# Performance work log

Hardware: AMD Instinct MI355X
Metric: run time of the kernel (lower is better)

Reference implementation:

```python
import jax, jax.numpy as jnp
import numpy as np

ETA = 0.1
DT = 1.0
H, DH = 8, 64


def setup_inputs() -> dict:
    key = jax.random.key(0)
    ks = jax.random.split(key, 7)
    B, N, D = 4, 2048, 1024
    s = 0.02
    return {
        "x": jax.random.normal(ks[0], (B, N, D), dtype=jnp.float32),
        "gamma": jax.random.uniform(ks[1], (B, N), dtype=jnp.float32),
        "state": jnp.zeros((B, H, DH, DH), dtype=jnp.float32),
        "Wq": (jax.random.normal(ks[2], (D, H * DH), dtype=jnp.float32) * s),
        "Wk": (jax.random.normal(ks[3], (D, H * DH), dtype=jnp.float32) * s),
        "Wv": (jax.random.normal(ks[4], (D, H * DH), dtype=jnp.float32) * s),
        "Wo": (jax.random.normal(ks[5], (H * DH, D), dtype=jnp.float32) * s),
        "bo": jnp.zeros((D,), dtype=jnp.float32),
    }


def reference(x, gamma, state, Wq, Wk, Wv, Wo, bo):
    B, N, D = x.shape
    # projections -> (N, B, H, DH) for scan over time
    q = (x @ Wq).reshape(B, N, H, DH).transpose(1, 0, 2, 3)
    k = (x @ Wk).reshape(B, N, H, DH).transpose(1, 0, 2, 3)
    v = (x @ Wv).reshape(B, N, H, DH).transpose(1, 0, 2, 3)
    # decay = exp(-clamp(gamma*dt, max=10)) -> (N, B)
    decay = jnp.exp(-jnp.minimum(gamma * DT, 10.0)).T

    def step(st, inp):
        q_t, k_t, v_t, d_t = inp  # (B,H,DH),(B,H,DH),(B,H,DH),(B,)
        # W_new = exp(-Gamma*dt) * stop_grad(W_old) + eta * k^T v
        st_new = d_t[:, None, None, None] * jax.lax.stop_gradient(st) \
                 + ETA * jnp.einsum('bhi,bhj->bhij', k_t, v_t)
        y_t = jnp.einsum('bhij,bhj->bhi', st_new, q_t)  # (B,H,DH)
        return st_new, y_t

    state_final, ys = jax.lax.scan(step, state, (q, k, v, decay))
    # ys: (N, B, H, DH) -> (B, N, H*DH)
    y = ys.transpose(1, 0, 2, 3).reshape(B, N, H * DH)
    out = y @ Wo + bo
    return out, state_final
```

## Files before the change

kernel.cpp:

```cpp
#include <hip/hip_runtime.h>

#define ETA 0.1f
#define BATCH 4
#define SEQ 2048
#define DMODEL 1024
#define NH 8
#define DHEAD 64
#define HD 512
#define QKVW 1536
#define CH 64
#define NCH (SEQ / CH)

typedef float f32x4 __attribute__((ext_vector_type(4)));
typedef short short8 __attribute__((ext_vector_type(8)));
typedef short short4v __attribute__((ext_vector_type(4)));

static __device__ __forceinline__ ushort f2bf(float f) {
  union { float f; unsigned u; } x; x.f = f;
  unsigned r = (x.u + 0x7fffu + ((x.u >> 16) & 1u)) >> 16;
  return (ushort)r;
}
static __device__ __forceinline__ float bf2f(ushort u) {
  union { unsigned u; float f; } x; x.u = ((unsigned)u) << 16;
  return x.f;
}

#define GLDS16(g, l)                                                    \
  __builtin_amdgcn_global_load_lds(                                     \
      (const __attribute__((address_space(1))) unsigned int*)(const void*)(g), \
      (__attribute__((address_space(3))) unsigned int*)(void*)(l), 16, 0, 0)

__global__ __launch_bounds__(256) void convx_kernel(
    const float* __restrict__ x, ushort* __restrict__ xb) {
  size_t i = ((size_t)blockIdx.x * 256 + threadIdx.x) * 16;
  ushort t[16];
#pragma unroll
  for (int u = 0; u < 4; ++u) {
    f32x4 v = *(const f32x4*)&x[i + u * 4];
#pragma unroll
    for (int e = 0; e < 4; ++e) t[u * 4 + e] = f2bf(v[e]);
  }
  *(short8*)&xb[i] = *(short8*)&t[0];
  *(short8*)&xb[i + 8] = *(short8*)&t[8];
}

__global__ __launch_bounds__(256) void convw_kernel(
    const float* __restrict__ Wq, const float* __restrict__ Wk,
    const float* __restrict__ Wv, const float* __restrict__ Wo,
    ushort* __restrict__ Wt, ushort* __restrict__ Wot) {
  const int m = blockIdx.y;
  const int bx = blockIdx.x;
  const int tid = threadIdx.x;
  __shared__ float T[32][33];

  const float* src;
  ushort* dst;
  int srcN, dstK, k0, n0, rowOff;
  if (m < 3) {
    src = (m == 0) ? Wq : ((m == 1) ? Wk : Wv);
    srcN = 512; dstK = 1024;
    k0 = (bx >> 4) << 5; n0 = (bx & 15) << 5;
    dst = Wt; rowOff = m * 512;
  } else {
    src = Wo; srcN = 1024; dstK = 512;
    k0 = (bx >> 5) << 5; n0 = (bx & 31) << 5;
    dst = Wot; rowOff = 0;
  }
  const int r = tid >> 3, c4 = (tid & 7) << 2;
  f32x4 v = *(const f32x4*)&src[(size_t)(k0 + r) * srcN + n0 + c4];
  T[r][c4 + 0] = v[0]; T[r][c4 + 1] = v[1];
  T[r][c4 + 2] = v[2]; T[r][c4 + 3] = v[3];
  __syncthreads();
  short4v o;
#pragma unroll
  for (int e = 0; e < 4; ++e) o[e] = (short)f2bf(T[c4 + e][r]);
  *(short4v*)&dst[(size_t)(rowOff + n0 + r) * dstK + k0 + c4] = o;
}

template <bool OUT_BF16>
__global__ __launch_bounds__(256, 3) void gemm_bt_kernel(
    const ushort* __restrict__ A, const ushort* __restrict__ Bt,
    void* __restrict__ Cv, const float* __restrict__ bias,
    int M, int N, int K) {
  const int tiles_n = N >> 7;
  const int nwg = gridDim.x;
  const int bid = blockIdx.x;
  const int swz = (bid & 7) * (nwg >> 3) + (bid >> 3);
  const int bm = swz / tiles_n;
  const int bn = swz % tiles_n;
  const int tid = threadIdx.x;
  const int w = tid >> 6, lane = tid & 63;
  const int wr = w >> 1, wc = w & 1;
  const int fr = lane & 15, fq = lane >> 4;

  __shared__ ushort As[3][128][32];
  __shared__ ushort Bs[3][128][32];

  f32x4 acc[4][4];
#pragma unroll
  for (int mi = 0; mi < 4; ++mi)
#pragma unroll
    for (int ni = 0; ni < 4; ++ni) acc[mi][ni] = f32x4{0.f, 0.f, 0.f, 0.f};

  const int lw = lane >> 2;
  const int scz = ((lane & 3) ^ ((lane >> 3) & 3)) << 3;
  const ushort* ga = A + (size_t)(bm * 128 + w * 32 + lw) * K + scz;
  const ushort* gb = Bt + (size_t)(bn * 128 + w * 32 + lw) * K + scz;
  const size_t rstep = (size_t)16 * K;

  const int nt = K >> 5;

#pragma unroll
  for (int pt = 0; pt < 2; ++pt) {
    ushort* la = &As[pt][w * 32][0];
    ushort* lb = &Bs[pt][w * 32][0];
    GLDS16(ga + pt * 32, la);
    GLDS16(ga + pt * 32 + rstep, la + 512);
    GLDS16(gb + pt * 32, lb);
    GLDS16(gb + pt * 32 + rstep, lb + 512);
  }

  const int fqs8 = (fq ^ ((fr >> 1) & 3)) * 8;

  for (int t = 0; t < nt; ++t) {
    if (t < nt - 1) {
      asm volatile("s_waitcnt vmcnt(4) lgkmcnt(0)\n\ts_barrier" ::: "memory");
    } else {
      asm volatile("s_waitcnt vmcnt(0) lgkmcnt(0)\n\ts_barrier" ::: "memory");
    }
    if (t + 2 < nt) {
      const int sb = (t + 2) % 3;
      const int kt = (t + 2) << 5;
      ushort* la = &As[sb][w * 32][0];
      ushort* lb = &Bs[sb][w * 32][0];
      GLDS16(ga + kt, la);
      GLDS16(ga + kt + rstep, la + 512);
      GLDS16(gb + kt, lb);
      GLDS16(gb + kt + rstep, lb + 512);
    }
    const int cb = t % 3;
    short8 a[4], b[4];
#pragma unroll
    for (int mi = 0; mi < 4; ++mi)
      a[mi] = *(const short8*)&As[cb][wr * 64 + mi * 16 + fr][fqs8];
#pragma unroll
    for (int ni = 0; ni < 4; ++ni)
      b[ni] = *(const short8*)&Bs[cb][wc * 64 + ni * 16 + fr][fqs8];
#pragma unroll
    for (int mi = 0; mi < 4; ++mi)
#pragma unroll
      for (int ni = 0; ni < 4; ++ni)
        acc[mi][ni] = __builtin_amdgcn_mfma_f32_16x16x32_bf16(
            a[mi], b[ni], acc[mi][ni], 0, 0, 0);
  }

#pragma unroll
  for (int ni = 0; ni < 4; ++ni) {
    const int gc = bn * 128 + wc * 64 + ni * 16 + fr;
    float badd = (!OUT_BF16 && bias) ? bias[gc] : 0.f;
#pragma unroll
    for (int mi = 0; mi < 4; ++mi) {
#pragma unroll
      for (int r = 0; r < 4; ++r) {
        const int gr = bm * 128 + wr * 64 + mi * 16 + fq * 4 + r;
        if (OUT_BF16) {
          ((ushort*)Cv)[(size_t)gr * N + gc] = f2bf(acc[mi][ni][r]);
        } else {
          ((float*)Cv)[(size_t)gr * N + gc] = acc[mi][ni][r] + badd;
        }
      }
    }
  }
}

__global__ __launch_bounds__(256) void intra_kernel(
    const ushort* __restrict__ qkv, const float* __restrict__ gamma,
    ushort* __restrict__ ybf, ushort* __restrict__ S, float* __restrict__ clb) {
  const int bx = blockIdx.x;
  const int c = bx & (NCH - 1);
  const int h = (bx >> 5) & (NH - 1);
  const int b = bx >> 8;
  const int tid = threadIdx.x;
  const int w = tid >> 6, lane = tid & 63;
  const int fr = lane & 15, fq = lane >> 4;

  __shared__ ushort Qs[64][72];
  __shared__ ushort Vs[64][72];
  __shared__ ushort KT[64][72];
  __shared__ ushort VT[64][72];
  __shared__ ushort Ps[64][72];
  __shared__ float cumS[64];
  __shared__ float clS;

  const int p = tid >> 2, d0 = (tid & 3) * 16;
  const ushort* base = &qkv[((size_t)b * SEQ + c * CH + p) * QKVW + h * 64 + d0];
  short8 q0 = *(const short8*)base;
  short8 q1 = *(const short8*)(base + 8);
  short8 k0 = *(const short8*)(base + 512);
  short8 k1 = *(const short8*)(base + 520);
  short8 v0 = *(const short8*)(base + 1024);
  short8 v1 = *(const short8*)(base + 1032);

  if (tid < 64) {
    float g = gamma[(size_t)b * SEQ + c * CH + tid];
    float prod = expf(-fminf(g, 10.f));
#pragma unroll
    for (int off = 1; off < 64; off <<= 1) {
      float o = __shfl_up(prod, off);
      if (tid >= off) prod *= o;
    }
    cumS[tid] = prod;
    if (tid == 63) clS = prod;
  }
  __syncthreads();

  {
    const float cp = cumS[p];
    const float rc = 1.f / cp;
    ushort tq[16], tv[16];
#pragma unroll
    for (int j = 0; j < 8; ++j) {
      tq[j]     = f2bf(bf2f((ushort)q0[j]) * cp);
      tq[8 + j] = f2bf(bf2f((ushort)q1[j]) * cp);
      tv[j]     = f2bf(bf2f((ushort)v0[j]) * rc);
      tv[8 + j] = f2bf(bf2f((ushort)v1[j]) * rc);
      KT[d0 + j][p] = (ushort)k0[j];
      KT[d0 + 8 + j][p] = (ushort)k1[j];
      VT[d0 + j][p] = tv[j];
      VT[d0 + 8 + j][p] = tv[8 + j];
    }
    *(short8*)&Qs[p][d0] = *(short8*)&tq[0];
    *(short8*)&Qs[p][d0 + 8] = *(short8*)&tq[8];
    *(short8*)&Vs[p][d0] = *(short8*)&tv[0];
    *(short8*)&Vs[p][d0 + 8] = *(short8*)&tv[8];
  }
  __syncthreads();

  const int arow = w * 16 + fr;
  {
    short8 a0 = *(const short8*)&Qs[arow][fq * 8];
    short8 a1 = *(const short8*)&Qs[arow][32 + fq * 8];
#pragma unroll
    for (int cf = 0; cf < 4; ++cf) {
      f32x4 acc = {0.f, 0.f, 0.f, 0.f};
      if (cf <= w) {
        short8 b0 = *(const short8*)&Vs[cf * 16 + fr][fq * 8];
        short8 b1 = *(const short8*)&Vs[cf * 16 + fr][32 + fq * 8];
        acc = __builtin_amdgcn_mfma_f32_16x16x32_bf16(a0, b0, acc, 0, 0, 0);
        acc = __builtin_amdgcn_mfma_f32_16x16x32_bf16(a1, b1, acc, 0, 0, 0);
      }
#pragma unroll
      for (int r = 0; r < 4; ++r) {
        int pi = w * 16 + fq * 4 + r, si = cf * 16 + fr;
        Ps[pi][si] = f2bf((si <= pi) ? acc[r] * ETA : 0.f);
      }
    }
  }
  __syncthreads();

  {
    short8 p0 = *(const short8*)&Ps[arow][fq * 8];
    short8 p1 = *(const short8*)&Ps[arow][32 + fq * 8];
    short8 ka0 = *(const short8*)&KT[arow][fq * 8];
    short8 ka1 = *(const short8*)&KT[arow][32 + fq * 8];
    const float scl = ETA * clS;
    const size_t yrow0 = (size_t)b * SEQ + c * CH;
    ushort* Sp = &S[(((size_t)(b * NH + h)) * NCH + c) << 12];
#pragma unroll
    for (int cf = 0; cf < 4; ++cf) {
      short8 bk0 = *(const short8*)&KT[cf * 16 + fr][fq * 8];
      short8 bk1 = *(const short8*)&KT[cf * 16 + fr][32 + fq * 8];
      f32x4 accY = {0.f, 0.f, 0.f, 0.f};
      accY = __builtin_amdgcn_mfma_f32_16x16x32_bf16(p0, bk0, accY, 0, 0, 0);
      accY = __builtin_amdgcn_mfma_f32_16x16x32_bf16(p1, bk1, accY, 0, 0, 0);
      short8 bv0 = *(const short8*)&VT[cf * 16 + fr][fq * 8];
      short8 bv1 = *(const short8*)&VT[cf * 16 + fr][32 + fq * 8];
      f32x4 accS = {0.f, 0.f, 0.f, 0.f};
      accS = __builtin_amdgcn_mfma_f32_16x16x32_bf16(ka0, bv0, accS, 0, 0, 0);
      accS = __builtin_amdgcn_mfma_f32_16x16x32_bf16(ka1, bv1, accS, 0, 0, 0);
#pragma unroll
      for (int r = 0; r < 4; ++r) {
        int row = w * 16 + fq * 4 + r;
        int col = cf * 16 + fr;
        ybf[(yrow0 + row) * HD + h * 64 + col] = f2bf(accY[r]);
        Sp[row * 64 + col] = f2bf(accS[r] * scl);
      }
    }
  }
  if (tid == 0 && h == 0) clb[b * NCH + c] = clS;
}

__global__ __launch_bounds__(256) void prop_kernel(
    const float* __restrict__ state0, const ushort* __restrict__ S,
    const float* __restrict__ clb, ushort* __restrict__ stash,
    float* __restrict__ state_out) {
  const int bh = blockIdx.x >> 2, rg = blockIdx.x & 3;
  const int b = bh >> 3;
  const int tid = threadIdx.x;
  const int i = rg * 16 + (tid >> 4);
  const int j0 = (tid & 15) * 4;
  const size_t off = ((size_t)bh * 64 + i) * 64 + j0;
  const size_t coff = (size_t)i * 64 + j0;

  f32x4 st = *(const f32x4*)&state0[off];
#pragma unroll 4
  for (int c = 0; c < NCH; ++c) {
    const size_t base = (((size_t)bh * NCH + c) << 12) + coff;
    short4v sv;
#pragma unroll
    for (int e = 0; e < 4; ++e) sv[e] = (short)f2bf(st[e]);
    *(short4v*)&stash[base] = sv;
    short4v s = *(const short4v*)&S[base];
    float clv = clb[b * NCH + c];
#pragma unroll
    for (int e = 0; e < 4; ++e) st[e] = st[e] * clv + bf2f((ushort)s[e]);
  }
  *(f32x4*)&state_out[off] = st;
}

__global__ __launch_bounds__(256) void inter_kernel(
    const ushort* __restrict__ qkv, const float* __restrict__ gamma,
    const ushort* __restrict__ stash, ushort* __restrict__ ybf) {
  const int bx = blockIdx.x;
  const int c = bx & (NCH - 1);
  const int h = (bx >> 5) & (NH - 1);
  const int b = bx >> 8;
  const int tid = threadIdx.x;
  const int w = tid >> 6, lane = tid & 63;
  const int fr = lane & 15, fq = lane >> 4;

  __shared__ ushort Qs[64][72];
  __shared__ ushort Bs[64][72];
  __shared__ float cumS[64];

  const int p = tid >> 2, d0 = (tid & 3) * 16;
  const ushort* qp = &qkv[((size_t)b * SEQ + c * CH + p) * QKVW + h * 64 + d0];
  short8 q0 = *(const short8*)qp;
  short8 q1 = *(const short8*)(qp + 8);
  const size_t sb = ((((size_t)(b * NH + h)) * NCH + c) << 12) + (size_t)p * 64 + d0;
  short8 s0 = *(const short8*)&stash[sb];
  short8 s1 = *(const short8*)&stash[sb + 8];

  if (tid < 64) {
    float g = gamma[(size_t)b * SEQ + c * CH + tid];
    float prod = expf(-fminf(g, 10.f));
#pragma unroll
    for (int off = 1; off < 64; off <<= 1) {
      float o = __shfl_up(prod, off);
      if (tid >= off) prod *= o;
    }
    cumS[tid] = prod;
  }
  __syncthreads();

  {
    const float cp = cumS[p];
    ushort tq[16];
#pragma unroll
    for (int j = 0; j < 8; ++j) {
      tq[j]     = f2bf(bf2f((ushort)q0[j]) * cp);
      tq[8 + j] = f2bf(bf2f((ushort)q1[j]) * cp);
    }
    *(short8*)&Qs[p][d0] = *(short8*)&tq[0];
    *(short8*)&Qs[p][d0 + 8] = *(short8*)&tq[8];
    *(short8*)&Bs[p][d0] = s0;
    *(short8*)&Bs[p][d0 + 8] = s1;
  }
  __syncthreads();

  const int arow = w * 16 + fr;
  short8 a0 = *(const short8*)&Qs[arow][fq * 8];
  short8 a1 = *(const short8*)&Qs[arow][32 + fq * 8];
  const size_t yrow0 = (size_t)b * SEQ + c * CH;
#pragma unroll
  for (int cf = 0; cf < 4; ++cf) {
    short8 b0 = *(const short8*)&Bs[cf * 16 + fr][fq * 8];
    short8 b1 = *(const short8*)&Bs[cf * 16 + fr][32 + fq * 8];
    f32x4 acc = {0.f, 0.f, 0.f, 0.f};
    acc = __builtin_amdgcn_mfma_f32_16x16x32_bf16(a0, b0, acc, 0, 0, 0);
    acc = __builtin_amdgcn_mfma_f32_16x16x32_bf16(a1, b1, acc, 0, 0, 0);
#pragma unroll
    for (int r = 0; r < 4; ++r) {
      int row = w * 16 + fq * 4 + r;
      int col = cf * 16 + fr;
      size_t idx = (yrow0 + row) * HD + h * 64 + col;
      ybf[idx] = f2bf(bf2f(ybf[idx]) + acc[r]);
    }
  }
}

extern "C" void kernel_launch(void* const* d_in, const int* in_sizes, int n_in,
                              void* d_out, int out_size, void* d_ws, size_t ws_size,
                              hipStream_t stream) {
  const float* x      = (const float*)d_in[0];
  const float* gamma  = (const float*)d_in[1];
  const float* state0 = (const float*)d_in[2];
  const float* Wq     = (const float*)d_in[3];
  const float* Wk     = (const float*)d_in[4];
  const float* Wv     = (const float*)d_in[5];
  const float* Wo     = (const float*)d_in[6];
  const float* bo     = (const float*)d_in[7];

  float* out = (float*)d_out;
  float* state_out = out + (size_t)BATCH * SEQ * DMODEL;

  const int M = BATCH * SEQ;

  ushort* xb  = (ushort*)d_ws;
  ushort* wt  = xb + (size_t)M * DMODEL;
  ushort* wot = wt + (size_t)QKVW * DMODEL;
  ushort* qkv = wot + (size_t)DMODEL * HD;
  ushort* ybf = qkv + (size_t)M * QKVW;
  ushort* Sb  = ybf + (size_t)M * HD;
  ushort* stash = Sb + (size_t)BATCH * NH * NCH * 4096;
  float*  clb   = (float*)(stash + (size_t)BATCH * NH * NCH * 4096);

  dim3 blk(256);

  convx_kernel<<<dim3((M * DMODEL) / (256 * 16)), blk, 0, stream>>>(x, xb);
  convw_kernel<<<dim3(512, 4), blk, 0, stream>>>(Wq, Wk, Wv, Wo, wt, wot);

  gemm_bt_kernel<true><<<dim3((M / 128) * (QKVW / 128)), blk, 0, stream>>>(
      xb, wt, qkv, nullptr, M, QKVW, DMODEL);

  intra_kernel<<<dim3(BATCH * NH * NCH), blk, 0, stream>>>(
      qkv, gamma, ybf, Sb, clb);
  prop_kernel<<<dim3(BATCH * NH * 4), blk, 0, stream>>>(
      state0, Sb, clb, stash, state_out);
  inter_kernel<<<dim3(BATCH * NH * NCH), blk, 0, stream>>>(
      qkv, gamma, stash, ybf);

  gemm_bt_kernel<false><<<dim3((M / 128) * (DMODEL / 128)), blk, 0, stream>>>(
      ybf, wot, out, bo, M, DMODEL, HD);
}
```

Measured before the change: 96.70 us.

## Move intra-chunk output into inter kernel and merge conversion kernels

```diff
diff --git a/kernel.cpp b/kernel.cpp
--- a/kernel.cpp
+++ b/kernel.cpp
@@ -30,29 +30,29 @@
       (const __attribute__((address_space(1))) unsigned int*)(const void*)(g), \
       (__attribute__((address_space(3))) unsigned int*)(void*)(l), 16, 0, 0)
 
-__global__ __launch_bounds__(256) void convx_kernel(
-    const float* __restrict__ x, ushort* __restrict__ xb) {
-  size_t i = ((size_t)blockIdx.x * 256 + threadIdx.x) * 16;
-  ushort t[16];
-#pragma unroll
-  for (int u = 0; u < 4; ++u) {
-    f32x4 v = *(const f32x4*)&x[i + u * 4];
-#pragma unroll
-    for (int e = 0; e < 4; ++e) t[u * 4 + e] = f2bf(v[e]);
-  }
-  *(short8*)&xb[i] = *(short8*)&t[0];
-  *(short8*)&xb[i + 8] = *(short8*)&t[8];
-}
-
-__global__ __launch_bounds__(256) void convw_kernel(
-    const float* __restrict__ Wq, const float* __restrict__ Wk,
-    const float* __restrict__ Wv, const float* __restrict__ Wo,
+__global__ __launch_bounds__(256) void conv_kernel(
+    const float* __restrict__ x, const float* __restrict__ Wq,
+    const float* __restrict__ Wk, const float* __restrict__ Wv,
+    const float* __restrict__ Wo, ushort* __restrict__ xb,
     ushort* __restrict__ Wt, ushort* __restrict__ Wot) {
-  const int m = blockIdx.y;
-  const int bx = blockIdx.x;
   const int tid = threadIdx.x;
   __shared__ float T[32][33];
-
+  if (blockIdx.x < 2048) {
+    size_t i = ((size_t)blockIdx.x * 256 + tid) * 16;
+    ushort t[16];
+#pragma unroll
+    for (int u = 0; u < 4; ++u) {
+      f32x4 v = *(const f32x4*)&x[i + u * 4];
+#pragma unroll
+      for (int e = 0; e < 4; ++e) t[u * 4 + e] = f2bf(v[e]);
+    }
+    *(short8*)&xb[i] = *(short8*)&t[0];
+    *(short8*)&xb[i + 8] = *(short8*)&t[8];
+    return;
+  }
+  const int idx = blockIdx.x - 2048;
+  const int m = idx >> 9;
+  const int bx = idx & 511;
   const float* src;
   ushort* dst;
   int srcN, dstK, k0, n0, rowOff;
@@ -173,9 +173,9 @@
   }
 }
 
-__global__ __launch_bounds__(256) void intra_kernel(
+__global__ __launch_bounds__(256) void intraS_kernel(
     const ushort* __restrict__ qkv, const float* __restrict__ gamma,
-    ushort* __restrict__ ybf, ushort* __restrict__ S, float* __restrict__ clb) {
+    ushort* __restrict__ S, float* __restrict__ clb) {
   const int bx = blockIdx.x;
   const int c = bx & (NCH - 1);
   const int h = (bx >> 5) & (NH - 1);
@@ -184,110 +184,61 @@
   const int w = tid >> 6, lane = tid & 63;
   const int fr = lane & 15, fq = lane >> 4;
 
-  __shared__ ushort Qs[64][72];
-  __shared__ ushort Vs[64][72];
   __shared__ ushort KT[64][72];
   __shared__ ushort VT[64][72];
-  __shared__ ushort Ps[64][72];
   __shared__ float cumS[64];
-  __shared__ float clS;
 
   const int p = tid >> 2, d0 = (tid & 3) * 16;
   const ushort* base = &qkv[((size_t)b * SEQ + c * CH + p) * QKVW + h * 64 + d0];
-  short8 q0 = *(const short8*)base;
-  short8 q1 = *(const short8*)(base + 8);
   short8 k0 = *(const short8*)(base + 512);
   short8 k1 = *(const short8*)(base + 520);
   short8 v0 = *(const short8*)(base + 1024);
   short8 v1 = *(const short8*)(base + 1032);
 
-  if (tid < 64) {
-    float g = gamma[(size_t)b * SEQ + c * CH + tid];
+  {
+    float g = gamma[(size_t)b * SEQ + c * CH + lane];
     float prod = expf(-fminf(g, 10.f));
 #pragma unroll
     for (int off = 1; off < 64; off <<= 1) {
       float o = __shfl_up(prod, off);
-      if (tid >= off) prod *= o;
-    }
-    cumS[tid] = prod;
-    if (tid == 63) clS = prod;
+      if (lane >= off) prod *= o;
+    }
+    cumS[lane] = prod;
   }
   __syncthreads();
 
   {
-    const float cp = cumS[p];
-    const float rc = 1.f / cp;
-    ushort tq[16], tv[16];
+    const float rc = 1.f / cumS[p];
 #pragma unroll
     for (int j = 0; j < 8; ++j) {
-      tq[j]     = f2bf(bf2f((ushort)q0[j]) * cp);
-      tq[8 + j] = f2bf(bf2f((ushort)q1[j]) * cp);
-      tv[j]     = f2bf(bf2f((ushort)v0[j]) * rc);
-      tv[8 + j] = f2bf(bf2f((ushort)v1[j]) * rc);
       KT[d0 + j][p] = (ushort)k0[j];
       KT[d0 + 8 + j][p] = (ushort)k1[j];
-      VT[d0 + j][p] = tv[j];
-      VT[d0 + 8 + j][p] = tv[8 + j];
-    }
-    *(short8*)&Qs[p][d0] = *(short8*)&tq[0];
-    *(short8*)&Qs[p][d0 + 8] = *(short8*)&tq[8];
-    *(short8*)&Vs[p][d0] = *(short8*)&tv[0];
-    *(short8*)&Vs[p][d0 + 8] = *(short8*)&tv[8];
-  }
-  __syncthreads();
-
+      VT[d0 + j][p] = f2bf(bf2f((ushort)v0[j]) * rc);
+      VT[d0 + 8 + j][p] = f2bf(bf2f((ushort)v1[j]) * rc);
+    }
+  }
+  __syncthreads();
+
+  const float scl = ETA * cumS[63];
   const int arow = w * 16 + fr;
-  {
-    short8 a0 = *(const short8*)&Qs[arow][fq * 8];
-    short8 a1 = *(const short8*)&Qs[arow][32 + fq * 8];
-#pragma unroll
-    for (int cf = 0; cf < 4; ++cf) {
-      f32x4 acc = {0.f, 0.f, 0.f, 0.f};
-      if (cf <= w) {
-        short8 b0 = *(const short8*)&Vs[cf * 16 + fr][fq * 8];
-        short8 b1 = *(const short8*)&Vs[cf * 16 + fr][32 + fq * 8];
-        acc = __builtin_amdgcn_mfma_f32_16x16x32_bf16(a0, b0, acc, 0, 0, 0);
-        acc = __builtin_amdgcn_mfma_f32_16x16x32_bf16(a1, b1, acc, 0, 0, 0);
-      }
-#pragma unroll
-      for (int r = 0; r < 4; ++r) {
-        int pi = w * 16 + fq * 4 + r, si = cf * 16 + fr;
-        Ps[pi][si] = f2bf((si <= pi) ? acc[r] * ETA : 0.f);
-      }
-    }
-  }
-  __syncthreads();
-
-  {
-    short8 p0 = *(const short8*)&Ps[arow][fq * 8];
-    short8 p1 = *(const short8*)&Ps[arow][32 + fq * 8];
-    short8 ka0 = *(const short8*)&KT[arow][fq * 8];
-    short8 ka1 = *(const short8*)&KT[arow][32 + fq * 8];
-    const float scl = ETA * clS;
-    const size_t yrow0 = (size_t)b * SEQ + c * CH;
-    ushort* Sp = &S[(((size_t)(b * NH + h)) * NCH + c) << 12];
-#pragma unroll
-    for (int cf = 0; cf < 4; ++cf) {
-      short8 bk0 = *(const short8*)&KT[cf * 16 + fr][fq * 8];
-      short8 bk1 = *(const short8*)&KT[cf * 16 + fr][32 + fq * 8];
-      f32x4 accY = {0.f, 0.f, 0.f, 0.f};
-      accY = __builtin_amdgcn_mfma_f32_16x16x32_bf16(p0, bk0, accY, 0, 0, 0);
-      accY = __builtin_amdgcn_mfma_f32_16x16x32_bf16(p1, bk1, accY, 0, 0, 0);
-      short8 bv0 = *(const short8*)&VT[cf * 16 + fr][fq * 8];
-      short8 bv1 = *(const short8*)&VT[cf * 16 + fr][32 + fq * 8];
-      f32x4 accS = {0.f, 0.f, 0.f, 0.f};
-      accS = __builtin_amdgcn_mfma_f32_16x16x32_bf16(ka0, bv0, accS, 0, 0, 0);
-      accS = __builtin_amdgcn_mfma_f32_16x16x32_bf16(ka1, bv1, accS, 0, 0, 0);
-#pragma unroll
-      for (int r = 0; r < 4; ++r) {
-        int row = w * 16 + fq * 4 + r;
-        int col = cf * 16 + fr;
-        ybf[(yrow0 + row) * HD + h * 64 + col] = f2bf(accY[r]);
-        Sp[row * 64 + col] = f2bf(accS[r] * scl);
-      }
-    }
-  }
-  if (tid == 0 && h == 0) clb[b * NCH + c] = clS;
+  short8 ka0 = *(const short8*)&KT[arow][fq * 8];
+  short8 ka1 = *(const short8*)&KT[arow][32 + fq * 8];
+  ushort* Sp = &S[(((size_t)(b * NH + h)) * NCH + c) << 12];
+#pragma unroll
+  for (int cf = 0; cf < 4; ++cf) {
+    short8 bv0 = *(const short8*)&VT[cf * 16 + fr][fq * 8];
+    short8 bv1 = *(const short8*)&VT[cf * 16 + fr][32 + fq * 8];
+    f32x4 accS = {0.f, 0.f, 0.f, 0.f};
+    accS = __builtin_amdgcn_mfma_f32_16x16x32_bf16(ka0, bv0, accS, 0, 0, 0);
+    accS = __builtin_amdgcn_mfma_f32_16x16x32_bf16(ka1, bv1, accS, 0, 0, 0);
+#pragma unroll
+    for (int r = 0; r < 4; ++r) {
+      int row = w * 16 + fq * 4 + r;
+      int col = cf * 16 + fr;
+      Sp[row * 64 + col] = f2bf(accS[r] * scl);
+    }
+  }
+  if (tid == 0 && h == 0) clb[b * NCH + c] = cumS[63];
 }
 
 __global__ __launch_bounds__(256) void prop_kernel(
@@ -318,7 +269,7 @@
   *(f32x4*)&state_out[off] = st;
 }
 
-__global__ __launch_bounds__(256) void inter_kernel(
+__global__ __launch_bounds__(256) void intraY_kernel(
     const ushort* __restrict__ qkv, const float* __restrict__ gamma,
     const ushort* __restrict__ stash, ushort* __restrict__ ybf) {
   const int bx = blockIdx.x;
@@ -330,61 +281,98 @@
   const int fr = lane & 15, fq = lane >> 4;
 
   __shared__ ushort Qs[64][72];
-  __shared__ ushort Bs[64][72];
+  __shared__ ushort Vs[64][72];
+  __shared__ ushort KT[64][72];
+  __shared__ ushort Ps[64][72];
+  __shared__ ushort Bst[64][72];
   __shared__ float cumS[64];
 
   const int p = tid >> 2, d0 = (tid & 3) * 16;
-  const ushort* qp = &qkv[((size_t)b * SEQ + c * CH + p) * QKVW + h * 64 + d0];
-  short8 q0 = *(const short8*)qp;
-  short8 q1 = *(const short8*)(qp + 8);
+  const ushort* base = &qkv[((size_t)b * SEQ + c * CH + p) * QKVW + h * 64 + d0];
+  short8 q0 = *(const short8*)base;
+  short8 q1 = *(const short8*)(base + 8);
+  short8 k0 = *(const short8*)(base + 512);
+  short8 k1 = *(const short8*)(base + 520);
+  short8 v0 = *(const short8*)(base + 1024);
+  short8 v1 = *(const short8*)(base + 1032);
   const size_t sb = ((((size_t)(b * NH + h)) * NCH + c) << 12) + (size_t)p * 64 + d0;
   short8 s0 = *(const short8*)&stash[sb];
   short8 s1 = *(const short8*)&stash[sb + 8];
 
-  if (tid < 64) {
-    float g = gamma[(size_t)b * SEQ + c * CH + tid];
+  {
+    float g = gamma[(size_t)b * SEQ + c * CH + lane];
     float prod = expf(-fminf(g, 10.f));
 #pragma unroll
     for (int off = 1; off < 64; off <<= 1) {
       float o = __shfl_up(prod, off);
-      if (tid >= off) prod *= o;
-    }
-    cumS[tid] = prod;
+      if (lane >= off) prod *= o;
+    }
+    cumS[lane] = prod;
   }
   __syncthreads();
 
   {
     const float cp = cumS[p];
-    ushort tq[16];
+    const float rc = 1.f / cp;
+    ushort tq[16], tv[16];
 #pragma unroll
     for (int j = 0; j < 8; ++j) {
       tq[j]     = f2bf(bf2f((ushort)q0[j]) * cp);
       tq[8 + j] = f2bf(bf2f((ushort)q1[j]) * cp);
+      tv[j]     = f2bf(bf2f((ushort)v0[j]) * rc);
+      tv[8 + j] = f2bf(bf2f((ushort)v1[j]) * rc);
+      KT[d0 + j][p] = (ushort)k0[j];
+      KT[d0 + 8 + j][p] = (ushort)k1[j];
     }
     *(short8*)&Qs[p][d0] = *(short8*)&tq[0];
     *(short8*)&Qs[p][d0 + 8] = *(short8*)&tq[8];
-    *(short8*)&Bs[p][d0] = s0;
-    *(short8*)&Bs[p][d0 + 8] = s1;
+    *(short8*)&Vs[p][d0] = *(short8*)&tv[0];
+    *(short8*)&Vs[p][d0 + 8] = *(short8*)&tv[8];
+    *(short8*)&Bst[p][d0] = s0;
+    *(short8*)&Bst[p][d0 + 8] = s1;
   }
   __syncthreads();
 
   const int arow = w * 16 + fr;
   short8 a0 = *(const short8*)&Qs[arow][fq * 8];
   short8 a1 = *(const short8*)&Qs[arow][32 + fq * 8];
+
+#pragma unroll
+  for (int cf = 0; cf < 4; ++cf) {
+    f32x4 acc = {0.f, 0.f, 0.f, 0.f};
+    if (cf <= w) {
+      short8 b0 = *(const short8*)&Vs[cf * 16 + fr][fq * 8];
+      short8 b1 = *(const short8*)&Vs[cf * 16 + fr][32 + fq * 8];
+      acc = __builtin_amdgcn_mfma_f32_16x16x32_bf16(a0, b0, acc, 0, 0, 0);
+      acc = __builtin_amdgcn_mfma_f32_16x16x32_bf16(a1, b1, acc, 0, 0, 0);
+    }
+#pragma unroll
+    for (int r = 0; r < 4; ++r) {
+      int pi = w * 16 + fq * 4 + r, si = cf * 16 + fr;
+      Ps[pi][si] = f2bf((si <= pi) ? acc[r] * ETA : 0.f);
+    }
+  }
+  __syncthreads();
+
+  short8 p0 = *(const short8*)&Ps[arow][fq * 8];
+  short8 p1 = *(const short8*)&Ps[arow][32 + fq * 8];
   const size_t yrow0 = (size_t)b * SEQ + c * CH;
 #pragma unroll
   for (int cf = 0; cf < 4; ++cf) {
-    short8 b0 = *(const short8*)&Bs[cf * 16 + fr][fq * 8];
-    short8 b1 = *(const short8*)&Bs[cf * 16 + fr][32 + fq * 8];
-    f32x4 acc = {0.f, 0.f, 0.f, 0.f};
-    acc = __builtin_amdgcn_mfma_f32_16x16x32_bf16(a0, b0, acc, 0, 0, 0);
-    acc = __builtin_amdgcn_mfma_f32_16x16x32_bf16(a1, b1, acc, 0, 0, 0);
+    f32x4 accY = {0.f, 0.f, 0.f, 0.f};
+    short8 bs0 = *(const short8*)&Bst[cf * 16 + fr][fq * 8];
+    short8 bs1 = *(const short8*)&Bst[cf * 16 + fr][32 + fq * 8];
+    accY = __builtin_amdgcn_mfma_f32_16x16x32_bf16(a0, bs0, accY, 0, 0, 0);
+    accY = __builtin_amdgcn_mfma_f32_16x16x32_bf16(a1, bs1, accY, 0, 0, 0);
+    short8 bk0 = *(const short8*)&KT[cf * 16 + fr][fq * 8];
+    short8 bk1 = *(const short8*)&KT[cf * 16 + fr][32 + fq * 8];
+    accY = __builtin_amdgcn_mfma_f32_16x16x32_bf16(p0, bk0, accY, 0, 0, 0);
+    accY = __builtin_amdgcn_mfma_f32_16x16x32_bf16(p1, bk1, accY, 0, 0, 0);
 #pragma unroll
     for (int r = 0; r < 4; ++r) {
       int row = w * 16 + fq * 4 + r;
       int col = cf * 16 + fr;
-      size_t idx = (yrow0 + row) * HD + h * 64 + col;
-      ybf[idx] = f2bf(bf2f(ybf[idx]) + acc[r]);
+      ybf[(yrow0 + row) * HD + h * 64 + col] = f2bf(accY[r]);
     }
   }
 }
@@ -417,17 +405,16 @@
 
   dim3 blk(256);
 
-  convx_kernel<<<dim3((M * DMODEL) / (256 * 16)), blk, 0, stream>>>(x, xb);
-  convw_kernel<<<dim3(512, 4), blk, 0, stream>>>(Wq, Wk, Wv, Wo, wt, wot);
+  conv_kernel<<<dim3(4096), blk, 0, stream>>>(x, Wq, Wk, Wv, Wo, xb, wt, wot);
 
   gemm_bt_kernel<true><<<dim3((M / 128) * (QKVW / 128)), blk, 0, stream>>>(
       xb, wt, qkv, nullptr, M, QKVW, DMODEL);
 
-  intra_kernel<<<dim3(BATCH * NH * NCH), blk, 0, stream>>>(
-      qkv, gamma, ybf, Sb, clb);
+  intraS_kernel<<<dim3(BATCH * NH * NCH), blk, 0, stream>>>(
+      qkv, gamma, Sb, clb);
   prop_kernel<<<dim3(BATCH * NH * 4), blk, 0, stream>>>(
       state0, Sb, clb, stash, state_out);
-  inter_kernel<<<dim3(BATCH * NH * NCH), blk, 0, stream>>>(
+  intraY_kernel<<<dim3(BATCH * NH * NCH), blk, 0, stream>>>(
       qkv, gamma, stash, ybf);
 
   gemm_bt_kernel<false><<<dim3((M / 128) * (DMODEL / 128)), blk, 0, stream>>>(
```

Result: faster. 92.39 us (-4.5%).
